# Performance work log

Hardware: AMD Instinct MI355X
Metric: run time of the kernel (lower is better)

The kernel has to match this reference:

```python
import jax, jax.numpy as jnp
import numpy as np

B, S, D, H = 2, 2048, 768, 12
HD = D // H


def setup_inputs() -> dict:
    key = jax.random.key(0)
    ks = jax.random.split(key, 11)
    scale = 1.0 / np.sqrt(D)
    return {
        "query": jax.random.normal(ks[0], (B, S, D), jnp.float32),
        "key_": jax.random.normal(ks[1], (B, S, D), jnp.float32),
        "value": jax.random.normal(ks[2], (B, S, D), jnp.float32),
        "Wq": jax.random.normal(ks[3], (D, D), jnp.float32) * scale,
        "bq": jnp.zeros((D,), jnp.float32),
        "Wk": jax.random.normal(ks[4], (D, D), jnp.float32) * scale,
        "bk": jnp.zeros((D,), jnp.float32),
        "Wv": jax.random.normal(ks[5], (D, D), jnp.float32) * scale,
        "bv": jnp.zeros((D,), jnp.float32),
        "Wo": jax.random.normal(ks[6], (D, D), jnp.float32) * scale,
        "bo": jnp.zeros((D,), jnp.float32),
    }


def reference(query, key_, value, Wq, bq, Wk, bk, Wv, bv, Wo, bo):
    # Linear projections (W stored as [in, out]); dropout = identity (eval)
    def split_heads(x):
        # [B, S, D] -> [B, H, S, HD]
        return x.reshape(B, S, H, HD).transpose(0, 2, 1, 3)

    Q = split_heads(query @ Wq + bq)
    K = split_heads(key_ @ Wk + bk)
    V = split_heads(value @ Wv + bv)

    inv_sqrt_dk = 1.0 / jnp.sqrt(jnp.asarray(HD, Q.dtype))
    score = jnp.einsum("bhqd,bhkd->bhqk", Q, K) * inv_sqrt_dk  # [B,H,S,S]
    prob = jax.nn.softmax(score, axis=-1)  # source bug: mask is never applied
    out = jnp.einsum("bhqk,bhkd->bhqd", prob, V)  # [B,H,S,HD]
    out = out.transpose(0, 2, 1, 3).reshape(B, S, D)
    return out @ Wo + bo
```

## Files before the change

kernel.cpp:

```cpp
#include <hip/hip_runtime.h>
#include <hip/hip_bf16.h>

#define BB 2
#define SS 2048
#define DDIM 768
#define NH 12
#define HD 64
#define MTOT (BB*SS)

constexpr float QSCALE = 0.125f * 1.44269504088896340736f;

typedef __bf16 bf16_t;
typedef __bf16 bf16x8 __attribute__((ext_vector_type(8)));
typedef __bf16 bf16x4 __attribute__((ext_vector_type(4)));
typedef float  f32x4  __attribute__((ext_vector_type(4)));

static __device__ __forceinline__ f32x4 mfma16(bf16x8 a, bf16x8 b, f32x4 c) {
    return __builtin_amdgcn_mfma_f32_16x16x32_bf16(a, b, c, 0, 0, 0);
}

typedef __attribute__((address_space(3))) unsigned int lds_u32;
typedef __attribute__((address_space(1))) const unsigned int glob_u32;
static __device__ __forceinline__ void gload16(const bf16_t* g, bf16_t* l) {
    __builtin_amdgcn_global_load_lds((glob_u32*)g, (lds_u32*)l, 16, 0, 0);
}

__global__ __launch_bounds__(256) void prep_w(
    const float* __restrict__ Wq, const float* __restrict__ Wk,
    const float* __restrict__ Wv, const float* __restrict__ Wo,
    bf16_t* __restrict__ Wt)
{
    const int z = blockIdx.z, tid = threadIdx.x;
    __shared__ float tile[32][33];
    const float* W = (z == 0) ? Wq : (z == 1) ? Wk : (z == 2) ? Wv : Wo;
    int n0 = blockIdx.x * 32, k0 = blockIdx.y * 32;
    int tx = tid & 31, ty = tid >> 5;
#pragma unroll
    for (int i = 0; i < 4; i++) {
        int k = ty + i * 8;
        tile[k][tx] = W[(size_t)(k0 + k) * DDIM + n0 + tx];
    }
    __syncthreads();
    bf16_t* out = Wt + (size_t)z * DDIM * DDIM;
#pragma unroll
    for (int i = 0; i < 4; i++) {
        int n = ty + i * 8;
        out[(size_t)(n0 + n) * DDIM + k0 + tx] = (bf16_t)tile[tx][n];
    }
}

__global__ __launch_bounds__(256) void gemm_qkv(
    const float* __restrict__ qf32, const float* __restrict__ kf32,
    const float* __restrict__ vf,
    const float* __restrict__ bq, const float* __restrict__ bk, const float* __restrict__ bv,
    const bf16_t* __restrict__ Wt,
    bf16_t* __restrict__ Q, bf16_t* __restrict__ K, bf16_t* __restrict__ Vtg)
{
    __shared__ alignas(16) bf16_t As[64 * 64];
    __shared__ alignas(16) bf16_t Bs[128 * 64];
    const int gid = blockIdx.x;
    const int lid = (gid & 7) * 144 + (gid >> 3);
    const int z   = lid / 384;
    const int rem = lid - z * 384;
    const int mi  = rem / 6, ni = rem - mi * 6;
    const int m0 = mi * 64, n0 = ni * 128;

    const int tid = threadIdx.x, lane = tid & 63, w = tid >> 6;
    const int wm = (w >> 1) * 32, wn = (w & 1) * 64;
    const int quad = lane >> 4, l15 = lane & 15;

    const float* Af = (z == 0) ? qf32 : (z == 1) ? kf32 : vf;
    const bf16_t* Bt = Wt + (size_t)z * (DDIM * DDIM);
    const int arow = lane >> 3;
    const int asl  = ((lane & 7) ^ arow) * 8;
    bf16_t* BsW = &Bs[w * 2048];
    const int frow = tid >> 2, fq = tid & 3;
    const int rsw = frow & 7;
    const float* Abase = Af + (size_t)(m0 + frow) * DDIM + fq * 16;

    f32x4 acc[2][4];
#pragma unroll
    for (int mt = 0; mt < 2; mt++)
#pragma unroll
        for (int nt = 0; nt < 4; nt++) { f32x4 zz = {0.f,0.f,0.f,0.f}; acc[mt][nt] = zz; }

    f32x4 vA[4];
#pragma unroll
    for (int i = 0; i < 4; i++) vA[i] = *(const f32x4*)(Abase + 4 * i);

    for (int k0 = 0; k0 < DDIM; k0 += 64) {
        __syncthreads();
#pragma unroll
        for (int j = 0; j < 2; j++) {
            bf16x8 oj;
#pragma unroll
            for (int e = 0; e < 4; e++) {
                oj[e]     = (bf16_t)vA[2 * j][e];
                oj[e + 4] = (bf16_t)vA[2 * j + 1][e];
            }
            int phys = (fq * 2 + j) ^ rsw;
            *(bf16x8*)&As[frow * 64 + phys * 8] = oj;
        }
        {
            const bf16_t* Bg = Bt + (size_t)(n0 + w * 32 + arow) * DDIM + k0 + asl;
#pragma unroll
            for (int i = 0; i < 4; i++)
                gload16(Bg + (size_t)(8 * i) * DDIM, BsW + 512 * i);
        }
        __syncthreads();
        if (k0 + 64 < DDIM) {
            const float* nsrc = Abase + k0 + 64;
#pragma unroll
            for (int i = 0; i < 4; i++) vA[i] = *(const f32x4*)(nsrc + 4 * i);
        }
#pragma unroll
        for (int h = 0; h < 2; h++) {
            bf16x8 a[2], b[4];
#pragma unroll
            for (int mt = 0; mt < 2; mt++) {
                int r = wm + mt * 16 + l15;
                a[mt] = *(const bf16x8*)&As[r * 64 + (((h * 4 + quad) ^ (r & 7)) * 8)];
            }
#pragma unroll
            for (int nt = 0; nt < 4; nt++) {
                int r = wn + nt * 16 + l15;
                b[nt] = *(const bf16x8*)&Bs[r * 64 + (((h * 4 + quad) ^ (r & 7)) * 8)];
            }
#pragma unroll
            for (int mt = 0; mt < 2; mt++)
#pragma unroll
                for (int nt = 0; nt < 4; nt++)
                    acc[mt][nt] = mfma16(a[mt], b[nt], acc[mt][nt]);
        }
    }

    const float* bias = (z == 0) ? bq : (z == 1) ? bk : bv;
    float bvals[4];
#pragma unroll
    for (int nt = 0; nt < 4; nt++)
        bvals[nt] = bias[n0 + wn + nt * 16 + l15];

    if (z == 2) {
#pragma unroll
        for (int mt = 0; mt < 2; mt++) {
            int row0 = m0 + wm + mt * 16 + quad * 4;
#pragma unroll
            for (int nt = 0; nt < 4; nt++) {
                int col = n0 + wn + nt * 16 + l15;
                bf16x4 pk;
#pragma unroll
                for (int r = 0; r < 4; r++) pk[r] = (bf16_t)(acc[mt][nt][r] + bvals[nt]);
                *(bf16x4*)&Vtg[(size_t)col * MTOT + row0] = pk;
            }
        }
    } else {
        bf16_t* C = (z == 0) ? Q : K;
        float scale = (z == 0) ? QSCALE : 1.0f;
#pragma unroll
        for (int mt = 0; mt < 2; mt++) {
            int row0 = m0 + wm + mt * 16 + quad * 4;
#pragma unroll
            for (int nt = 0; nt < 4; nt++) {
                int col = n0 + wn + nt * 16 + l15;
#pragma unroll
                for (int r = 0; r < 4; r++)
                    C[(size_t)(row0 + r) * DDIM + col] = (bf16_t)((acc[mt][nt][r] + bvals[nt]) * scale);
            }
        }
    }
}

__global__ __launch_bounds__(256) void gemm_out(
    const bf16_t* __restrict__ Ab, const bf16_t* __restrict__ Bt,
    const float* __restrict__ bo, float* __restrict__ out)
{
    __shared__ alignas(16) bf16_t As[64 * 64];
    __shared__ alignas(16) bf16_t Bs[64 * 64];
    const int gid = blockIdx.x;
    const int lid = (gid & 7) * 96 + (gid >> 3);
    const int mi  = lid / 12, ni = lid - mi * 12;
    const int m0 = mi * 64, n0 = ni * 64;

    const int tid = threadIdx.x, lane = tid & 63, w = tid >> 6;
    const int wm = (w >> 1) * 32, wn = (w & 1) * 32;
    const int quad = lane >> 4, l15 = lane & 15;
    const int arow = lane >> 3;
    const int asl  = ((lane & 7) ^ arow) * 8;
    bf16_t* AsW = &As[w * 1024];
    bf16_t* BsW = &Bs[w * 1024];

    f32x4 acc[2][2];
#pragma unroll
    for (int mt = 0; mt < 2; mt++)
#pragma unroll
        for (int nt = 0; nt < 2; nt++) { f32x4 zz = {0.f,0.f,0.f,0.f}; acc[mt][nt] = zz; }

    for (int k0 = 0; k0 < DDIM; k0 += 64) {
        __syncthreads();
        {
            const bf16_t* Ag = Ab + (size_t)(m0 + w * 16 + arow) * DDIM + k0 + asl;
            gload16(Ag, AsW);
            gload16(Ag + (size_t)8 * DDIM, AsW + 512);
            const bf16_t* Bg = Bt + (size_t)(n0 + w * 16 + arow) * DDIM + k0 + asl;
            gload16(Bg, BsW);
            gload16(Bg + (size_t)8 * DDIM, BsW + 512);
        }
        __syncthreads();

#pragma unroll
        for (int h = 0; h < 2; h++) {
            bf16x8 a[2], b[2];
#pragma unroll
            for (int mt = 0; mt < 2; mt++) {
                int r = wm + mt * 16 + l15;
                a[mt] = *(const bf16x8*)&As[r * 64 + (((h * 4 + quad) ^ (r & 7)) * 8)];
            }
#pragma unroll
            for (int nt = 0; nt < 2; nt++) {
                int r = wn + nt * 16 + l15;
                b[nt] = *(const bf16x8*)&Bs[r * 64 + (((h * 4 + quad) ^ (r & 7)) * 8)];
            }
#pragma unroll
            for (int mt = 0; mt < 2; mt++)
#pragma unroll
                for (int nt = 0; nt < 2; nt++)
                    acc[mt][nt] = mfma16(a[mt], b[nt], acc[mt][nt]);
        }
    }

    float bvals[2];
#pragma unroll
    for (int nt = 0; nt < 2; nt++)
        bvals[nt] = bo[n0 + wn + nt * 16 + l15];
#pragma unroll
    for (int mt = 0; mt < 2; mt++) {
        int row0 = m0 + wm + mt * 16 + quad * 4;
#pragma unroll
        for (int nt = 0; nt < 2; nt++) {
            int col = n0 + wn + nt * 16 + l15;
#pragma unroll
            for (int r = 0; r < 4; r++)
                out[(size_t)(row0 + r) * DDIM + col] = acc[mt][nt][r] + bvals[nt];
        }
    }
}

__global__ __launch_bounds__(256) void attn_kernel(
    const bf16_t* __restrict__ Qb, const bf16_t* __restrict__ Kb,
    const bf16_t* __restrict__ Vtg, bf16_t* __restrict__ Ab)
{
    const int id = blockIdx.x;
    const int hb = id % 24, qi = id / 24;
    const int h = hb % NH, b = hb / NH;
    const int q0 = qi * 64;
    const int tid = threadIdx.x, lane = tid & 63, w = tid >> 6;
    const int quad = lane >> 4, l15 = lane & 15;

    __shared__ union {
        struct {
            alignas(16) bf16_t Ps[64][144];
        } a;
        struct {
            alignas(16) float Obuf[2][64][68];
            float Lb[4][64];
        } m;
    } u;

    bf16x8 qf[4][2];
#pragma unroll
    for (int qt = 0; qt < 4; qt++) {
        const bf16_t* src = Qb + (size_t)(b * SS + q0 + qt * 16 + l15) * DDIM + h * HD;
#pragma unroll
        for (int kh = 0; kh < 2; kh++)
            qf[qt][kh] = *(const bf16x8*)(src + kh * 32 + quad * 8);
    }

    f32x4 o[4][4];
#pragma unroll
    for (int dt = 0; dt < 4; dt++)
#pragma unroll
        for (int qt = 0; qt < 4; qt++) { f32x4 z = {0.f,0.f,0.f,0.f}; o[dt][qt] = z; }
    float l_s[4];
#pragma unroll
    for (int qt = 0; qt < 4; qt++) l_s[qt] = 0.f;

    const bf16_t* kfrag = Kb + (size_t)(b * SS + w * 32 + l15) * DDIM + h * HD + quad * 8;
    const bf16_t* vfrag = Vtg + (size_t)(h * HD + l15) * MTOT + b * SS + w * 32 + quad * 8;

    for (int kt0 = 0; kt0 < SS; kt0 += 128) {
        f32x4 s_[2][4];
#pragma unroll
        for (int kt = 0; kt < 2; kt++) {
            const bf16_t* kr = kfrag + (size_t)(kt0 + kt * 16) * DDIM;
            bf16x8 ak0 = *(const bf16x8*)(kr);
            bf16x8 ak1 = *(const bf16x8*)(kr + 32);
#pragma unroll
            for (int qt = 0; qt < 4; qt++) {
                f32x4 z = {0.f,0.f,0.f,0.f};
                z = mfma16(ak0, qf[qt][0], z);
                z = mfma16(ak1, qf[qt][1], z);
                s_[kt][qt] = z;
            }
        }

#pragma unroll
        for (int qt = 0; qt < 4; qt++) {
            float rs = l_s[qt];
#pragma unroll
            for (int kt = 0; kt < 2; kt++) {
                bf16x4 pk;
#pragma unroll
                for (int r = 0; r < 4; r++) {
                    float p = __builtin_amdgcn_exp2f(s_[kt][qt][r]);
                    rs += p;
                    pk[r] = (bf16_t)p;
                }
                *(bf16x4*)&u.a.Ps[qt * 16 + l15][w * 32 + kt * 16 + quad * 4] = pk;
            }
            l_s[qt] = rs;
        }

        bf16x8 av8[4], bp[4];
#pragma unroll
        for (int dt = 0; dt < 4; dt++)
            av8[dt] = *(const bf16x8*)(vfrag + (size_t)(dt * 16) * MTOT + kt0);
#pragma unroll
        for (int qt = 0; qt < 4; qt++)
            bp[qt] = *(const bf16x8*)&u.a.Ps[qt * 16 + l15][w * 32 + quad * 8];
#pragma unroll
        for (int dt = 0; dt < 4; dt++)
#pragma unroll
            for (int qt = 0; qt < 4; qt++)
                o[dt][qt] = mfma16(av8[dt], bp[qt], o[dt][qt]);
    }

#pragma unroll
    for (int qt = 0; qt < 4; qt++) {
        float rs = l_s[qt];
        rs += __shfl_xor(rs, 16, 64);
        rs += __shfl_xor(rs, 32, 64);
        l_s[qt] = rs;
    }
    __syncthreads();
    if (quad == 0) {
#pragma unroll
        for (int qt = 0; qt < 4; qt++)
            u.m.Lb[w][qt * 16 + l15] = l_s[qt];
    }
    __syncthreads();
    float lstar[4];
#pragma unroll
    for (int qt = 0; qt < 4; qt++) {
        int q = qt * 16 + l15;
        lstar[qt] = u.m.Lb[0][q] + u.m.Lb[1][q] + u.m.Lb[2][q] + u.m.Lb[3][q];
    }
    if (w >= 2) {
        float* dst = &u.m.Obuf[w - 2][lane][0];
#pragma unroll
        for (int dt = 0; dt < 4; dt++)
#pragma unroll
            for (int qt = 0; qt < 4; qt++)
                *(f32x4*)(dst + (dt * 4 + qt) * 4) = o[dt][qt];
    }
    __syncthreads();
    if (w < 2) {
        const float* src = &u.m.Obuf[w][lane][0];
#pragma unroll
        for (int dt = 0; dt < 4; dt++)
#pragma unroll
            for (int qt = 0; qt < 4; qt++)
                o[dt][qt] += *(const f32x4*)(src + (dt * 4 + qt) * 4);
    }
    __syncthreads();
    if (w == 1) {
        float* dst = &u.m.Obuf[0][lane][0];
#pragma unroll
        for (int dt = 0; dt < 4; dt++)
#pragma unroll
            for (int qt = 0; qt < 4; qt++)
                *(f32x4*)(dst + (dt * 4 + qt) * 4) = o[dt][qt];
    }
    __syncthreads();
    if (w == 0) {
        const float* src = &u.m.Obuf[0][lane][0];
#pragma unroll
        for (int dt = 0; dt < 4; dt++)
#pragma unroll
            for (int qt = 0; qt < 4; qt++)
                o[dt][qt] += *(const f32x4*)(src + (dt * 4 + qt) * 4);
#pragma unroll
        for (int qt = 0; qt < 4; qt++) {
            float inv = 1.f / lstar[qt];
            size_t rbase = (size_t)(b * SS + q0 + qt * 16 + l15) * DDIM + h * HD;
#pragma unroll
            for (int dt = 0; dt < 4; dt++) {
                bf16x4 pk;
#pragma unroll
                for (int r = 0; r < 4; r++) pk[r] = (bf16_t)(o[dt][qt][r] * inv);
                *(bf16x4*)&Ab[rbase + dt * 16 + quad * 4] = pk;
            }
        }
    }
}

extern "C" void kernel_launch(void* const* d_in, const int* in_sizes, int n_in,
                              void* d_out, int out_size, void* d_ws, size_t ws_size,
                              hipStream_t stream)
{
    const float* q  = (const float*)d_in[0];
    const float* k  = (const float*)d_in[1];
    const float* v  = (const float*)d_in[2];
    const float* Wq = (const float*)d_in[3];
    const float* bq = (const float*)d_in[4];
    const float* Wk = (const float*)d_in[5];
    const float* bk = (const float*)d_in[6];
    const float* Wv = (const float*)d_in[7];
    const float* bv = (const float*)d_in[8];
    const float* Wo = (const float*)d_in[9];
    const float* bo = (const float*)d_in[10];
    float* out = (float*)d_out;

    bf16_t* Wt  = (bf16_t*)d_ws;
    bf16_t* Ab  = Wt + (size_t)4 * DDIM * DDIM;
    bf16_t* Qs  = Ab + (size_t)MTOT * DDIM;
    bf16_t* Ks  = Qs + (size_t)MTOT * DDIM;
    bf16_t* Vtg = Ks + (size_t)MTOT * DDIM;

    prep_w<<<dim3(24, 24, 4), 256, 0, stream>>>(Wq, Wk, Wv, Wo, Wt);
    gemm_qkv<<<dim3(1152), 256, 0, stream>>>(q, k, v, bq, bk, bv, Wt, Qs, Ks, Vtg);
    attn_kernel<<<dim3((SS / 64) * NH * BB), 256, 0, stream>>>(Qs, Ks, Vtg, Ab);
    gemm_out<<<dim3(768), 256, 0, stream>>>(Ab, Wt + (size_t)3 * DDIM * DDIM, bo, out);
}
```

Baseline: 197.9 us.

## Load GEMM MFMA operands directly from global memory, dropping LDS staging

Both the QKV projection GEMM and the output projection GEMM stop staging A/B tiles in shared memory and stop using async global-to-LDS loads and block barriers. Each wave now loads its MFMA fragments straight from global memory (through the caches) every 32-wide k step, converting fp32 A to bf16 in registers. This removes __syncthreads and LDS traffic, but data shared between waves in a block is now fetched redundantly from L1/L2, and the loads are narrower and less coalesced with no software prefetch.

```diff
diff --git a/kernel.cpp b/kernel.cpp
--- a/kernel.cpp
+++ b/kernel.cpp
@@ -19,12 +19,6 @@
     return __builtin_amdgcn_mfma_f32_16x16x32_bf16(a, b, c, 0, 0, 0);
 }
 
-typedef __attribute__((address_space(3))) unsigned int lds_u32;
-typedef __attribute__((address_space(1))) const unsigned int glob_u32;
-static __device__ __forceinline__ void gload16(const bf16_t* g, bf16_t* l) {
-    __builtin_amdgcn_global_load_lds((glob_u32*)g, (lds_u32*)l, 16, 0, 0);
-}
-
 __global__ __launch_bounds__(256) void prep_w(
     const float* __restrict__ Wq, const float* __restrict__ Wk,
     const float* __restrict__ Wv, const float* __restrict__ Wo,
@@ -56,8 +50,6 @@
     const bf16_t* __restrict__ Wt,
     bf16_t* __restrict__ Q, bf16_t* __restrict__ K, bf16_t* __restrict__ Vtg)
 {
-    __shared__ alignas(16) bf16_t As[64 * 64];
-    __shared__ alignas(16) bf16_t Bs[128 * 64];
     const int gid = blockIdx.x;
     const int lid = (gid & 7) * 144 + (gid >> 3);
     const int z   = lid / 384;
@@ -71,12 +63,9 @@
 
     const float* Af = (z == 0) ? qf32 : (z == 1) ? kf32 : vf;
     const bf16_t* Bt = Wt + (size_t)z * (DDIM * DDIM);
-    const int arow = lane >> 3;
-    const int asl  = ((lane & 7) ^ arow) * 8;
-    bf16_t* BsW = &Bs[w * 2048];
-    const int frow = tid >> 2, fq = tid & 3;
-    const int rsw = frow & 7;
-    const float* Abase = Af + (size_t)(m0 + frow) * DDIM + fq * 16;
+
+    const float*  ap = Af + (size_t)(m0 + wm + l15) * DDIM + quad * 8;
+    const bf16_t* bp = Bt + (size_t)(n0 + wn + l15) * DDIM + quad * 8;
 
     f32x4 acc[2][4];
 #pragma unroll
@@ -84,54 +73,24 @@
 #pragma unroll
         for (int nt = 0; nt < 4; nt++) { f32x4 zz = {0.f,0.f,0.f,0.f}; acc[mt][nt] = zz; }
 
-    f32x4 vA[4];
-#pragma unroll
-    for (int i = 0; i < 4; i++) vA[i] = *(const f32x4*)(Abase + 4 * i);
-
-    for (int k0 = 0; k0 < DDIM; k0 += 64) {
-        __syncthreads();
-#pragma unroll
-        for (int j = 0; j < 2; j++) {
-            bf16x8 oj;
-#pragma unroll
-            for (int e = 0; e < 4; e++) {
-                oj[e]     = (bf16_t)vA[2 * j][e];
-                oj[e + 4] = (bf16_t)vA[2 * j + 1][e];
-            }
-            int phys = (fq * 2 + j) ^ rsw;
-            *(bf16x8*)&As[frow * 64 + phys * 8] = oj;
-        }
-        {
-            const bf16_t* Bg = Bt + (size_t)(n0 + w * 32 + arow) * DDIM + k0 + asl;
-#pragma unroll
-            for (int i = 0; i < 4; i++)
-                gload16(Bg + (size_t)(8 * i) * DDIM, BsW + 512 * i);
-        }
-        __syncthreads();
-        if (k0 + 64 < DDIM) {
-            const float* nsrc = Abase + k0 + 64;
-#pragma unroll
-            for (int i = 0; i < 4; i++) vA[i] = *(const f32x4*)(nsrc + 4 * i);
-        }
-#pragma unroll
-        for (int h = 0; h < 2; h++) {
-            bf16x8 a[2], b[4];
-#pragma unroll
-            for (int mt = 0; mt < 2; mt++) {
-                int r = wm + mt * 16 + l15;
-                a[mt] = *(const bf16x8*)&As[r * 64 + (((h * 4 + quad) ^ (r & 7)) * 8)];
-            }
-#pragma unroll
-            for (int nt = 0; nt < 4; nt++) {
-                int r = wn + nt * 16 + l15;
-                b[nt] = *(const bf16x8*)&Bs[r * 64 + (((h * 4 + quad) ^ (r & 7)) * 8)];
-            }
-#pragma unroll
-            for (int mt = 0; mt < 2; mt++)
-#pragma unroll
-                for (int nt = 0; nt < 4; nt++)
-                    acc[mt][nt] = mfma16(a[mt], b[nt], acc[mt][nt]);
-        }
+    for (int k0 = 0; k0 < DDIM; k0 += 32) {
+        bf16x8 a[2], b[4];
+#pragma unroll
+        for (int mt = 0; mt < 2; mt++) {
+            const float* s = ap + (size_t)(mt * 16) * DDIM + k0;
+            f32x4 lo = *(const f32x4*)s;
+            f32x4 hi = *(const f32x4*)(s + 4);
+#pragma unroll
+            for (int e = 0; e < 4; e++) { a[mt][e] = (bf16_t)lo[e]; a[mt][e + 4] = (bf16_t)hi[e]; }
+        }
+#pragma unroll
+        for (int nt = 0; nt < 4; nt++)
+            b[nt] = *(const bf16x8*)(bp + (size_t)(nt * 16) * DDIM + k0);
+#pragma unroll
+        for (int mt = 0; mt < 2; mt++)
+#pragma unroll
+            for (int nt = 0; nt < 4; nt++)
+                acc[mt][nt] = mfma16(a[mt], b[nt], acc[mt][nt]);
     }
 
     const float* bias = (z == 0) ? bq : (z == 1) ? bk : bv;
@@ -174,8 +133,6 @@
     const bf16_t* __restrict__ Ab, const bf16_t* __restrict__ Bt,
     const float* __restrict__ bo, float* __restrict__ out)
 {
-    __shared__ alignas(16) bf16_t As[64 * 64];
-    __shared__ alignas(16) bf16_t Bs[64 * 64];
     const int gid = blockIdx.x;
     const int lid = (gid & 7) * 96 + (gid >> 3);
     const int mi  = lid / 12, ni = lid - mi * 12;
@@ -184,10 +141,9 @@
     const int tid = threadIdx.x, lane = tid & 63, w = tid >> 6;
     const int wm = (w >> 1) * 32, wn = (w & 1) * 32;
     const int quad = lane >> 4, l15 = lane & 15;
-    const int arow = lane >> 3;
-    const int asl  = ((lane & 7) ^ arow) * 8;
-    bf16_t* AsW = &As[w * 1024];
-    bf16_t* BsW = &Bs[w * 1024];
+
+    const bf16_t* apb = Ab + (size_t)(m0 + wm + l15) * DDIM + quad * 8;
+    const bf16_t* bpb = Bt + (size_t)(n0 + wn + l15) * DDIM + quad * 8;
 
     f32x4 acc[2][2];
 #pragma unroll
@@ -195,37 +151,19 @@
 #pragma unroll
         for (int nt = 0; nt < 2; nt++) { f32x4 zz = {0.f,0.f,0.f,0.f}; acc[mt][nt] = zz; }
 
-    for (int k0 = 0; k0 < DDIM; k0 += 64) {
-        __syncthreads();
-        {
-            const bf16_t* Ag = Ab + (size_t)(m0 + w * 16 + arow) * DDIM + k0 + asl;
-            gload16(Ag, AsW);
-            gload16(Ag + (size_t)8 * DDIM, AsW + 512);
-            const bf16_t* Bg = Bt + (size_t)(n0 + w * 16 + arow) * DDIM + k0 + asl;
-            gload16(Bg, BsW);
-            gload16(Bg + (size_t)8 * DDIM, BsW + 512);
-        }
-        __syncthreads();
-
-#pragma unroll
-        for (int h = 0; h < 2; h++) {
-            bf16x8 a[2], b[2];
-#pragma unroll
-            for (int mt = 0; mt < 2; mt++) {
-                int r = wm + mt * 16 + l15;
-                a[mt] = *(const bf16x8*)&As[r * 64 + (((h * 4 + quad) ^ (r & 7)) * 8)];
-            }
-#pragma unroll
-            for (int nt = 0; nt < 2; nt++) {
-                int r = wn + nt * 16 + l15;
-                b[nt] = *(const bf16x8*)&Bs[r * 64 + (((h * 4 + quad) ^ (r & 7)) * 8)];
-            }
-#pragma unroll
-            for (int mt = 0; mt < 2; mt++)
-#pragma unroll
-                for (int nt = 0; nt < 2; nt++)
-                    acc[mt][nt] = mfma16(a[mt], b[nt], acc[mt][nt]);
-        }
+    for (int k0 = 0; k0 < DDIM; k0 += 32) {
+        bf16x8 a[2], b[2];
+#pragma unroll
+        for (int mt = 0; mt < 2; mt++)
+            a[mt] = *(const bf16x8*)(apb + (size_t)(mt * 16) * DDIM + k0);
+#pragma unroll
+        for (int nt = 0; nt < 2; nt++)
+            b[nt] = *(const bf16x8*)(bpb + (size_t)(nt * 16) * DDIM + k0);
+#pragma unroll
+        for (int mt = 0; mt < 2; mt++)
+#pragma unroll
+            for (int nt = 0; nt < 2; nt++)
+                acc[mt][nt] = mfma16(a[mt], b[nt], acc[mt][nt]);
     }
 
     float bvals[2];
```

Result: slower. 293.8 us (+48.5%).
